# Kernel optimization log

Measured on AMD Instinct MI355X. Metric: run time of the kernel, lower is better.

Reference implementation:

```python
import jax, jax.numpy as jnp
import numpy as np

N = 8192
DIMS = [1024, 512, 256, 128]
ALPHA, BETA, ETA = 100.0, 1.0, 25.0


def setup_inputs() -> dict:
    key = jax.random.key(0)
    ks = jax.random.split(key, 20)
    X = jax.random.normal(ks[0], (N, DIMS[0]), dtype=jnp.float32)
    adj = (jax.random.uniform(ks[1], (N, N)) < 0.005).astype(jnp.float32)

    def xavier(k, fan_in, fan_out):
        lim = jnp.sqrt(6.0 / (fan_in + fan_out))
        return jax.random.uniform(k, (fan_in, fan_out), minval=-lim, maxval=lim, dtype=jnp.float32)

    # encoder GraphConv params
    W0 = xavier(ks[2], DIMS[0], DIMS[1]); b0 = jnp.zeros((DIMS[1],), jnp.float32)
    W1 = xavier(ks[3], DIMS[1], DIMS[2]); b1 = jnp.zeros((DIMS[2],), jnp.float32)
    W2 = xavier(ks[4], DIMS[2], DIMS[3]); b2 = jnp.zeros((DIMS[3],), jnp.float32)
    # attn_head params (out_sz = DIMS[2] = 256, input dim = DIMS[2])
    attn_W = jax.random.normal(ks[5], (DIMS[2], DIMS[2]), dtype=jnp.float32)  # [out_sz, D], used as seq @ W.T
    attn_a1 = jax.random.normal(ks[6], (DIMS[2],), dtype=jnp.float32)
    attn_a2 = jax.random.normal(ks[7], (DIMS[2],), dtype=jnp.float32)
    # decoder params (struct reversed: 128->256->512->1024)
    rd = DIMS[::-1]
    dW0 = jax.random.normal(ks[8], (rd[0], rd[1]), dtype=jnp.float32); db0 = jnp.zeros((rd[1],), jnp.float32)
    dW1 = jax.random.normal(ks[9], (rd[1], rd[2]), dtype=jnp.float32); db1 = jnp.zeros((rd[2],), jnp.float32)
    dW2 = jax.random.normal(ks[10], (rd[2], rd[3]), dtype=jnp.float32); db2 = jnp.zeros((rd[3],), jnp.float32)
    return {"X": X, "adj": adj, "W0": W0, "b0": b0, "W1": W1, "b1": b1, "W2": W2, "b2": b2,
            "attn_W": attn_W, "attn_a1": attn_a1, "attn_a2": attn_a2,
            "dW0": dW0, "db0": db0, "dW1": dW1, "db1": db1, "dW2": dW2, "db2": db2}


def reference(X, adj, W0, b0, W1, b1, W2, b2, attn_W, attn_a1, attn_a2,
              dW0, db0, dW1, db1, dW2, db2):
    lrelu = jax.nn.leaky_relu  # negative_slope=0.01, matches torch default

    # --- encode (dropout disabled / eval-mode) ---
    h = lrelu(adj @ (X @ W0) + b0)          # [N, 512]
    h = lrelu(adj @ (h @ W1) + b1)          # [N, 256]

    # GAT-style attn head (out_sz = 256)
    seq_fts = h @ attn_W.T                  # [N, 256]
    f1 = seq_fts @ attn_a1                  # [N]
    f2 = seq_fts @ attn_a2                  # [N]
    logits = f1[:, None] + f2[None, :]      # [N, N]
    mask = (adj > 0).astype(seq_fts.dtype)
    masked = lrelu(logits) - 1e9 * (1.0 - mask)
    coefs = jax.nn.softmax(masked, axis=-1)
    h = lrelu(coefs @ seq_fts)              # [N, 256]

    H = lrelu(adj @ (h @ W2) + b2)          # [N, 128]

    # --- decode ---
    Xr = jax.nn.sigmoid(H @ dW0 + db0)
    Xr = jax.nn.sigmoid(Xr @ dW1 + db1)
    Xr = jax.nn.sigmoid(Xr @ dW2 + db2)     # [N, 1024]

    # --- losses ---
    deg = adj.sum(axis=1)
    LH = deg[:, None] * H - adj @ H         # (D - A) @ H without materializing D
    loss_emb = 2.0 * jnp.sum(H * LH)
    B = X * (ETA - 1.0) + 1.0
    loss_res = jnp.sum(((Xr - X) * B) ** 2)
    loss = ALPHA * loss_res + BETA * loss_emb
    return loss, H, Xr
```

## Files before the change

kernel.cpp:

```cpp
#include <hip/hip_runtime.h>
#include <math.h>

#define NN 8192
#define ELL_W 128

typedef __attribute__((ext_vector_type(8))) short bf16x8;
typedef __attribute__((ext_vector_type(4))) float f32x4;

__device__ __forceinline__ float lrelu(float x) { return x > 0.f ? x : 0.01f * x; }
__device__ __forceinline__ unsigned short f2bf(float f) {
    unsigned u = __float_as_uint(f);
    return (unsigned short)((u + 0x7FFFu + ((u >> 16) & 1u)) >> 16);
}
__device__ __forceinline__ float bf2f(unsigned short h) { return __uint_as_float(((unsigned)h) << 16); }
__device__ __forceinline__ void split3(float v, unsigned short& h0, unsigned short& h1, unsigned short& h2) {
    h0 = f2bf(v); float r = v - bf2f(h0);
    h1 = f2bf(r); h2 = f2bf(r - bf2f(h1));
}

__device__ __forceinline__ void gload_lds16(const unsigned short* g, unsigned short* l) {
    __builtin_amdgcn_global_load_lds((const __attribute__((address_space(1))) unsigned int*)g,
                                     (__attribute__((address_space(3))) unsigned int*)l, 16, 0, 0);
}

__device__ __forceinline__ size_t a_plane_off(int rowg, int kg, int K) {
    int rr = rowg & 127, kk = kg & 31;
    int pc = (((kk >> 3) + (rr >> 1)) & 3);
    return ((size_t)(rowg >> 7) * (K >> 5) + (kg >> 5)) * 4096 + rr * 32 + pc * 8 + (kk & 7);
}

__global__ void build_ell_kernel(const float* __restrict__ adj, int* __restrict__ ell,
                                 int* __restrict__ cnt, float* __restrict__ deg) {
    const int row  = blockIdx.x * 4 + (threadIdx.x >> 6);
    const int lane = threadIdx.x & 63;
    const float4* arow = (const float4*)(adj + (size_t)row * NN);
    const unsigned long long lmask = (1ull << lane) - 1ull;
    int count = 0;
    for (int c0 = 0; c0 < NN; c0 += 256) {
        const float4 v = arow[(c0 >> 2) + lane];
        const int col = c0 + lane * 4;
        float f[4] = {v.x, v.y, v.z, v.w};
        #pragma unroll
        for (int q = 0; q < 4; ++q) {
            unsigned long long m = __ballot(f[q] > 0.f);
            if (f[q] > 0.f) {
                int pos = count + __popcll(m & lmask);
                if (pos < ELL_W) ell[row * ELL_W + pos] = col + q;
            }
            count += __popcll(m);
        }
    }
    if (lane == 0) {
        cnt[row] = count < ELL_W ? count : ELL_W;
        deg[row] = (float)count;
    }
}

__global__ void zero_accum_kernel(float* accum) { accum[0] = 0.f; accum[1] = 0.f; }

__global__ void splitA_kernel(const float* __restrict__ src, unsigned short* __restrict__ P0,
                              unsigned short* __restrict__ P1, unsigned short* __restrict__ P2,
                              int K, int nchunks) {
    int g = blockIdx.x * 256 + threadIdx.x;
    if (g >= nchunks) return;
    const int KT = K >> 5;
    int t = g >> 9, w = g & 511;
    int r = w >> 2, pc = w & 3;
    int c = (pc - (r >> 1)) & 3;
    int tm = t / KT, tk = t % KT;
    const float* s = src + (size_t)(tm * 128 + r) * K + tk * 32 + c * 8;
    const float4 v0 = *(const float4*)s, v1 = *(const float4*)(s + 4);
    float f[8] = {v0.x, v0.y, v0.z, v0.w, v1.x, v1.y, v1.z, v1.w};
    unsigned short a0[8], a1[8], a2[8];
    #pragma unroll
    for (int j = 0; j < 8; ++j) split3(f[j], a0[j], a1[j], a2[j]);
    *(uint4*)(P0 + (size_t)g * 8) = *(uint4*)a0;
    *(uint4*)(P1 + (size_t)g * 8) = *(uint4*)a1;
    *(uint4*)(P2 + (size_t)g * 8) = *(uint4*)a2;
}

__global__ void splitBT_kernel(const float* __restrict__ W, unsigned short* __restrict__ P0,
                               unsigned short* __restrict__ P1, unsigned short* __restrict__ P2,
                               int K, int N, int nchunks) {
    int g = blockIdx.x * 256 + threadIdx.x;
    if (g >= nchunks) return;
    const int KT = K >> 5;
    int t = g >> 8, w = g & 255;
    int r = w >> 2, pc = w & 3;
    int c = (pc - (r >> 1)) & 3;
    int tn = t / KT, tk = t % KT;
    const float* s = W + (size_t)(tk * 32 + c * 8) * N + tn * 64 + r;
    unsigned short a0[8], a1[8], a2[8];
    #pragma unroll
    for (int j = 0; j < 8; ++j) split3(s[(size_t)j * N], a0[j], a1[j], a2[j]);
    *(uint4*)(P0 + (size_t)g * 8) = *(uint4*)a0;
    *(uint4*)(P1 + (size_t)g * 8) = *(uint4*)a1;
    *(uint4*)(P2 + (size_t)g * 8) = *(uint4*)a2;
}

__global__ void splitBR_kernel(const float* __restrict__ W, unsigned short* __restrict__ P0,
                               unsigned short* __restrict__ P1, unsigned short* __restrict__ P2,
                               int K, int nchunks) {
    int g = blockIdx.x * 256 + threadIdx.x;
    if (g >= nchunks) return;
    const int KT = K >> 5;
    int t = g >> 8, w = g & 255;
    int r = w >> 2, pc = w & 3;
    int c = (pc - (r >> 1)) & 3;
    int tn = t / KT, tk = t % KT;
    const float* s = W + (size_t)(tn * 64 + r) * K + tk * 32 + c * 8;
    const float4 v0 = *(const float4*)s, v1 = *(const float4*)(s + 4);
    float f[8] = {v0.x, v0.y, v0.z, v0.w, v1.x, v1.y, v1.z, v1.w};
    unsigned short a0[8], a1[8], a2[8];
    #pragma unroll
    for (int j = 0; j < 8; ++j) split3(f[j], a0[j], a1[j], a2[j]);
    *(uint4*)(P0 + (size_t)g * 8) = *(uint4*)a0;
    *(uint4*)(P1 + (size_t)g * 8) = *(uint4*)a1;
    *(uint4*)(P2 + (size_t)g * 8) = *(uint4*)a2;
}

template <int ACT, int OUT>
__launch_bounds__(256)
__global__ void mfma_gemm_kernel(const unsigned short* __restrict__ A0, const unsigned short* __restrict__ A1,
                                 const unsigned short* __restrict__ A2,
                                 const unsigned short* __restrict__ B0, const unsigned short* __restrict__ B1,
                                 const unsigned short* __restrict__ B2,
                                 const float* __restrict__ bias, int K, int N,
                                 float* __restrict__ Cf,
                                 unsigned short* __restrict__ C0, unsigned short* __restrict__ C1,
                                 unsigned short* __restrict__ C2,
                                 const float* __restrict__ Xref, float* __restrict__ accum) {
    __shared__ __align__(16) unsigned short lds[18432];
    __shared__ float sred[256];
    const int tid = threadIdx.x, lane = tid & 63, wv = tid >> 6;
    const int KT = K >> 5;
    const int bm = blockIdx.y * 128, bn = blockIdx.x * 64;
    const int wr = (wv >> 1) * 64, wc = (wv & 1) * 32;
    const int lr = lane & 15, cch = lane >> 4;

    const unsigned short* Ap[3] = {A0 + (size_t)blockIdx.y * KT * 4096,
                                   A1 + (size_t)blockIdx.y * KT * 4096,
                                   A2 + (size_t)blockIdx.y * KT * 4096};
    const unsigned short* Bp[3] = {B0 + (size_t)blockIdx.x * KT * 2048,
                                   B1 + (size_t)blockIdx.x * KT * 2048,
                                   B2 + (size_t)blockIdx.x * KT * 2048};
    int offA[4], offB[2];
    #pragma unroll
    for (int mi = 0; mi < 4; ++mi) { int r = wr + mi * 16 + lr; offA[mi] = r * 32 + (((cch + (r >> 1)) & 3) << 3); }
    #pragma unroll
    for (int ni = 0; ni < 2; ++ni) { int r = wc + ni * 16 + lr; offB[ni] = r * 32 + (((cch + (r >> 1)) & 3) << 3); }

    f32x4 acc[4][2];
    #pragma unroll
    for (int i = 0; i < 4; ++i)
        #pragma unroll
        for (int j = 0; j < 2; ++j) acc[i][j] = (f32x4){0.f, 0.f, 0.f, 0.f};

    for (int tk = 0; tk < KT; ++tk) {
        #pragma unroll
        for (int i = 0; i < 6; ++i) {
            int s = i * 4 + wv, p = s >> 3, q = s & 7;
            gload_lds16(Ap[p] + (size_t)tk * 4096 + q * 512 + lane * 8, &lds[p * 4096 + q * 512]);
        }
        #pragma unroll
        for (int i = 0; i < 3; ++i) {
            int s = i * 4 + wv, p = s >> 2, q = s & 3;
            gload_lds16(Bp[p] + (size_t)tk * 2048 + q * 512 + lane * 8, &lds[12288 + p * 2048 + q * 512]);
        }
        __syncthreads();
        bf16x8 af[3][4], bfr[3][2];
        #pragma unroll
        for (int p = 0; p < 3; ++p) {
            #pragma unroll
            for (int mi = 0; mi < 4; ++mi) af[p][mi] = *(const bf16x8*)&lds[p * 4096 + offA[mi]];
            #pragma unroll
            for (int ni = 0; ni < 2; ++ni) bfr[p][ni] = *(const bf16x8*)&lds[12288 + p * 2048 + offB[ni]];
        }
        #pragma unroll
        for (int mi = 0; mi < 4; ++mi)
            #pragma unroll
            for (int ni = 0; ni < 2; ++ni) {
                f32x4 c = acc[mi][ni];
                c = __builtin_amdgcn_mfma_f32_16x16x32_bf16(af[0][mi], bfr[0][ni], c, 0, 0, 0);
                c = __builtin_amdgcn_mfma_f32_16x16x32_bf16(af[0][mi], bfr[1][ni], c, 0, 0, 0);
                c = __builtin_amdgcn_mfma_f32_16x16x32_bf16(af[1][mi], bfr[0][ni], c, 0, 0, 0);
                c = __builtin_amdgcn_mfma_f32_16x16x32_bf16(af[1][mi], bfr[1][ni], c, 0, 0, 0);
                c = __builtin_amdgcn_mfma_f32_16x16x32_bf16(af[0][mi], bfr[2][ni], c, 0, 0, 0);
                c = __builtin_amdgcn_mfma_f32_16x16x32_bf16(af[2][mi], bfr[0][ni], c, 0, 0, 0);
                acc[mi][ni] = c;
            }
        __syncthreads();
    }
    float local = 0.f;
    #pragma unroll
    for (int mi = 0; mi < 4; ++mi)
        #pragma unroll
        for (int ni = 0; ni < 2; ++ni) {
            const int colg = bn + wc + ni * 16 + lr;
            #pragma unroll
            for (int r = 0; r < 4; ++r) {
                const int rowg = bm + wr + mi * 16 + cch * 4 + r;
                float v = acc[mi][ni][r];
                if (ACT) { v += bias[colg]; v = 1.f / (1.f + __expf(-v)); }
                if (OUT == 0) {
                    Cf[(size_t)rowg * N + colg] = v;
                } else if (OUT == 1) {
                    size_t po = a_plane_off(rowg, colg, N);
                    unsigned short h0, h1, h2; split3(v, h0, h1, h2);
                    C0[po] = h0; C1[po] = h1; C2[po] = h2;
                } else {
                    const size_t o = (size_t)rowg * N + colg;
                    Cf[o] = v;
                    float x = Xref[o];
                    float d = (v - x) * fmaf(x, 24.f, 1.f);
                    local = fmaf(d, d, local);
                }
            }
        }
    if (OUT == 2) {
        sred[tid] = local; __syncthreads();
        for (int s = 128; s; s >>= 1) { if (tid < s) sred[tid] += sred[tid + s]; __syncthreads(); }
        if (tid == 0) atomicAdd(accum, sred[0]);
    }
}

template <int C, int OUTF, int OUTP>
__global__ void spmm_kernel(const float* __restrict__ M_, const int* __restrict__ ell,
                            const int* __restrict__ cnt, const float* __restrict__ bias,
                            float* __restrict__ out, float* __restrict__ out2,
                            unsigned short* __restrict__ P0, unsigned short* __restrict__ P1,
                            unsigned short* __restrict__ P2) {
    constexpr int TPR = C / 4;
    constexpr int RPB = 256 / TPR;
    const int rid = threadIdx.x / TPR;
    const int c4  = threadIdx.x % TPR;
    const int row = blockIdx.x * RPB + rid;
    __shared__ int nb_s[RPB][ELL_W];
    const int n = cnt[row];
    for (int t = c4; t < n; t += TPR) nb_s[rid][t] = ell[row * ELL_W + t];
    __syncthreads();
    float4 acc = {0.f, 0.f, 0.f, 0.f};
    for (int t = 0; t < n; ++t) {
        const float4 v = *(const float4*)(M_ + (size_t)nb_s[rid][t] * C + c4 * 4);
        acc.x += v.x; acc.y += v.y; acc.z += v.z; acc.w += v.w;
    }
    const float4 bv = *(const float4*)(bias + c4 * 4);
    float4 r;
    r.x = lrelu(acc.x + bv.x); r.y = lrelu(acc.y + bv.y);
    r.z = lrelu(acc.z + bv.z); r.w = lrelu(acc.w + bv.w);
    if (OUTF) {
        *(float4*)(out + (size_t)row * C + c4 * 4) = r;
        if (out2) {
            size_t o = (size_t)row * C + c4 * 4;
            out2[o] = r.x; out2[o + 1] = r.y; out2[o + 2] = r.z; out2[o + 3] = r.w;
        }
    }
    if (OUTP) {
        constexpr int KT = C >> 5;
        int tm = row >> 7, rr = row & 127;
        int tk = c4 >> 3, cc = (c4 >> 1) & 3, h = c4 & 1;
        int pc = (cc + (rr >> 1)) & 3;
        size_t off = ((size_t)tm * KT + tk) * 4096 + rr * 32 + pc * 8 + h * 4;
        ushort4 q0, q1, q2;
        split3(r.x, q0.x, q1.x, q2.x); split3(r.y, q0.y, q1.y, q2.y);
        split3(r.z, q0.z, q1.z, q2.z); split3(r.w, q0.w, q1.w, q2.w);
        *(ushort4*)(P0 + off) = q0; *(ushort4*)(P1 + off) = q1; *(ushort4*)(P2 + off) = q2;
    }
}

__global__ void f12_kernel(const float* __restrict__ seq, const float* __restrict__ a1,
                           const float* __restrict__ a2, float* __restrict__ f1,
                           float* __restrict__ f2) {
    const int row = blockIdx.x * 4 + (threadIdx.x >> 6);
    const int lane = threadIdx.x & 63;
    const float4 v  = *(const float4*)(seq + (size_t)row * 256 + lane * 4);
    const float4 w1 = *(const float4*)(a1 + lane * 4);
    const float4 w2 = *(const float4*)(a2 + lane * 4);
    float s1 = v.x * w1.x + v.y * w1.y + v.z * w1.z + v.w * w1.w;
    float s2 = v.x * w2.x + v.y * w2.y + v.z * w2.z + v.w * w2.w;
    #pragma unroll
    for (int o = 32; o; o >>= 1) { s1 += __shfl_xor(s1, o); s2 += __shfl_xor(s2, o); }
    if (lane == 0) { f1[row] = s1; f2[row] = s2; }
}

__global__ void attn_kernel(const float* __restrict__ seq, const int* __restrict__ ell,
                            const int* __restrict__ cnt, const float* __restrict__ f1,
                            const float* __restrict__ f2,
                            unsigned short* __restrict__ P0, unsigned short* __restrict__ P1,
                            unsigned short* __restrict__ P2) {
    const int wid = threadIdx.x >> 6, lane = threadIdx.x & 63;
    const int row = blockIdx.x * 4 + wid;
    __shared__ int   nb_s[4][ELL_W];
    __shared__ float cf_s[4][ELL_W];
    const int n = cnt[row];
    const float f1r = f1[row];
    float m = -3.0e38f;
    for (int t = lane; t < n; t += 64) {
        int j = ell[row * ELL_W + t];
        nb_s[wid][t] = j;
        float v = lrelu(f1r + f2[j]);
        cf_s[wid][t] = v;
        m = fmaxf(m, v);
    }
    #pragma unroll
    for (int o = 32; o; o >>= 1) m = fmaxf(m, __shfl_xor(m, o));
    __syncthreads();
    float s = 0.f;
    for (int t = lane; t < n; t += 64) {
        float e = __expf(cf_s[wid][t] - m);
        cf_s[wid][t] = e;
        s += e;
    }
    #pragma unroll
    for (int o = 32; o; o >>= 1) s += __shfl_xor(s, o);
    const float inv = 1.f / s;
    __syncthreads();
    float4 acc = {0.f, 0.f, 0.f, 0.f};
    for (int t = 0; t < n; ++t) {
        const float c = cf_s[wid][t];
        const float4 v = *(const float4*)(seq + (size_t)nb_s[wid][t] * 256 + lane * 4);
        acc.x = fmaf(c, v.x, acc.x); acc.y = fmaf(c, v.y, acc.y);
        acc.z = fmaf(c, v.z, acc.z); acc.w = fmaf(c, v.w, acc.w);
    }
    float4 r;
    r.x = lrelu(acc.x * inv); r.y = lrelu(acc.y * inv);
    r.z = lrelu(acc.z * inv); r.w = lrelu(acc.w * inv);
    int tm = row >> 7, rr = row & 127;
    int tk = lane >> 3, cc = (lane >> 1) & 3, h = lane & 1;
    int pc = (cc + (rr >> 1)) & 3;
    size_t off = ((size_t)tm * 8 + tk) * 4096 + rr * 32 + pc * 8 + h * 4;
    ushort4 q0, q1, q2;
    split3(r.x, q0.x, q1.x, q2.x); split3(r.y, q0.y, q1.y, q2.y);
    split3(r.z, q0.z, q1.z, q2.z); split3(r.w, q0.w, q1.w, q2.w);
    *(ushort4*)(P0 + off) = q0; *(ushort4*)(P1 + off) = q1; *(ushort4*)(P2 + off) = q2;
}

__global__ void loss_emb_kernel(const float* __restrict__ H, const int* __restrict__ ell,
                                const int* __restrict__ cnt, const float* __restrict__ deg,
                                float* __restrict__ accum) {
    const int row = blockIdx.x, tid = threadIdx.x;
    __shared__ int nb[ELL_W];
    __shared__ float sred[128];
    const int n = cnt[row];
    if (tid < n) nb[tid] = ell[row * ELL_W + tid];
    __syncthreads();
    float hv = H[(size_t)row * 128 + tid];
    float g = 0.f;
    for (int t = 0; t < n; ++t) g += H[(size_t)nb[t] * 128 + tid];
    float lh = deg[row] * hv - g;
    sred[tid] = hv * lh; __syncthreads();
    for (int s = 64; s; s >>= 1) { if (tid < s) sred[tid] += sred[tid + s]; __syncthreads(); }
    if (tid == 0) atomicAdd(accum + 1, sred[0]);
}

__global__ void finalize_kernel(const float* __restrict__ accum, float* __restrict__ out) {
    out[0] = 100.f * accum[0] + 2.f * accum[1];
}

extern "C" void kernel_launch(void* const* d_in, const int* in_sizes, int n_in,
                              void* d_out, int out_size, void* d_ws, size_t ws_size,
                              hipStream_t stream) {
    const float* X      = (const float*)d_in[0];
    const float* adj    = (const float*)d_in[1];
    const float* W0     = (const float*)d_in[2];
    const float* b0     = (const float*)d_in[3];
    const float* W1     = (const float*)d_in[4];
    const float* b1     = (const float*)d_in[5];
    const float* W2     = (const float*)d_in[6];
    const float* b2     = (const float*)d_in[7];
    const float* attn_W = (const float*)d_in[8];
    const float* a1     = (const float*)d_in[9];
    const float* a2     = (const float*)d_in[10];
    const float* dW0    = (const float*)d_in[11];
    const float* db0    = (const float*)d_in[12];
    const float* dW1    = (const float*)d_in[13];
    const float* db1    = (const float*)d_in[14];
    const float* dW2    = (const float*)d_in[15];
    const float* db2    = (const float*)d_in[16];

    float* out  = (float*)d_out;
    float* Hout = out + 1;
    float* Xr   = out + 1 + (size_t)NN * 128;

    char* w = (char*)d_ws;
    int*   ell   = (int*)w;   w += (size_t)NN * ELL_W * 4;
    int*   cnt   = (int*)w;   w += (size_t)NN * 4;
    float* deg   = (float*)w; w += (size_t)NN * 4;
    float* f1    = (float*)w; w += (size_t)NN * 4;
    float* f2    = (float*)w; w += (size_t)NN * 4;
    float* accum = (float*)w; w += 256;
    float* bufA  = (float*)w; w += (size_t)NN * 512 * 4;
    float* bufB  = (float*)w; w += (size_t)NN * 256 * 4;
    float* bufC  = (float*)w; w += (size_t)NN * 256 * 4;
    float* bufH  = (float*)w; w += (size_t)NN * 128 * 4;
    unsigned short *XP[3], *W0T[3], *h0P[3], *W1T[3], *h1P[3], *aWR[3], *h2P[3], *W2T[3];
    unsigned short *HP[3], *dW0T[3], *R0P[3], *dW1T[3], *R1P[3], *dW2T[3];
    for (int i = 0; i < 3; ++i) { XP[i]   = (unsigned short*)w; w += (size_t)NN * 1024 * 2; }
    for (int i = 0; i < 3; ++i) { W0T[i]  = (unsigned short*)w; w += (size_t)512 * 1024 * 2; }
    for (int i = 0; i < 3; ++i) { h0P[i]  = (unsigned short*)w; w += (size_t)NN * 512 * 2; }
    for (int i = 0; i < 3; ++i) { W1T[i]  = (unsigned short*)w; w += (size_t)256 * 512 * 2; }
    for (int i = 0; i < 3; ++i) { h1P[i]  = (unsigned short*)w; w += (size_t)NN * 256 * 2; }
    for (int i = 0; i < 3; ++i) { aWR[i]  = (unsigned short*)w; w += (size_t)256 * 256 * 2; }
    for (int i = 0; i < 3; ++i) { h2P[i]  = (unsigned short*)w; w += (size_t)NN * 256 * 2; }
    for (int i = 0; i < 3; ++i) { W2T[i]  = (unsigned short*)w; w += (size_t)128 * 256 * 2; }
    for (int i = 0; i < 3; ++i) { HP[i]   = (unsigned short*)w; w += (size_t)NN * 128 * 2; }
    for (int i = 0; i < 3; ++i) { dW0T[i] = (unsigned short*)w; w += (size_t)256 * 128 * 2; }
    for (int i = 0; i < 3; ++i) { R0P[i]  = (unsigned short*)w; w += (size_t)NN * 256 * 2; }
    for (int i = 0; i < 3; ++i) { dW1T[i] = (unsigned short*)w; w += (size_t)512 * 256 * 2; }
    for (int i = 0; i < 3; ++i) { R1P[i]  = (unsigned short*)w; w += (size_t)NN * 512 * 2; }
    for (int i = 0; i < 3; ++i) { dW2T[i] = (unsigned short*)w; w += (size_t)1024 * 512 * 2; }

    build_ell_kernel<<<dim3(NN / 4), dim3(256), 0, stream>>>(adj, ell, cnt, deg);
    zero_accum_kernel<<<1, 1, 0, stream>>>(accum);

    splitA_kernel<<<4096, 256, 0, stream>>>(X, XP[0], XP[1], XP[2], 1024, NN * 1024 / 8);
    splitBT_kernel<<<256, 256, 0, stream>>>(W0, W0T[0], W0T[1], W0T[2], 1024, 512, 512 * 1024 / 8);
    splitBT_kernel<<<64, 256, 0, stream>>>(W1, W1T[0], W1T[1], W1T[2], 512, 256, 256 * 512 / 8);
    splitBR_kernel<<<32, 256, 0, stream>>>(attn_W, aWR[0], aWR[1], aWR[2], 256, 256 * 256 / 8);
    splitBT_kernel<<<16, 256, 0, stream>>>(W2, W2T[0], W2T[1], W2T[2], 256, 128, 128 * 256 / 8);
    splitBT_kernel<<<16, 256, 0, stream>>>(dW0, dW0T[0], dW0T[1], dW0T[2], 128, 256, 256 * 128 / 8);
    splitBT_kernel<<<64, 256, 0, stream>>>(dW1, dW1T[0], dW1T[1], dW1T[2], 256, 512, 512 * 256 / 8);
    splitBT_kernel<<<256, 256, 0, stream>>>(dW2, dW2T[0], dW2T[1], dW2T[2], 512, 1024, 1024 * 512 / 8);

    mfma_gemm_kernel<0, 0><<<dim3(8, 64), 256, 0, stream>>>(
        XP[0], XP[1], XP[2], W0T[0], W0T[1], W0T[2], nullptr, 1024, 512,
        bufA, nullptr, nullptr, nullptr, nullptr, nullptr);
    spmm_kernel<512, 0, 1><<<NN / 2, 256, 0, stream>>>(bufA, ell, cnt, b0, nullptr, nullptr, h0P[0], h0P[1], h0P[2]);
    mfma_gemm_kernel<0, 0><<<dim3(4, 64), 256, 0, stream>>>(
        h0P[0], h0P[1], h0P[2], W1T[0], W1T[1], W1T[2], nullptr, 512, 256,
        bufC, nullptr, nullptr, nullptr, nullptr, nullptr);
    spmm_kernel<256, 0, 1><<<NN / 4, 256, 0, stream>>>(bufC, ell, cnt, b1, nullptr, nullptr, h1P[0], h1P[1], h1P[2]);
    mfma_gemm_kernel<0, 0><<<dim3(4, 64), 256, 0, stream>>>(
        h1P[0], h1P[1], h1P[2], aWR[0], aWR[1], aWR[2], nullptr, 256, 256,
        bufB, nullptr, nullptr, nullptr, nullptr, nullptr);
    f12_kernel<<<NN / 4, 256, 0, stream>>>(bufB, a1, a2, f1, f2);
    attn_kernel<<<NN / 4, 256, 0, stream>>>(bufB, ell, cnt, f1, f2, h2P[0], h2P[1], h2P[2]);
    mfma_gemm_kernel<0, 0><<<dim3(2, 64), 256, 0, stream>>>(
        h2P[0], h2P[1], h2P[2], W2T[0], W2T[1], W2T[2], nullptr, 256, 128,
        bufA, nullptr, nullptr, nullptr, nullptr, nullptr);
    spmm_kernel<128, 1, 1><<<NN / 8, 256, 0, stream>>>(bufA, ell, cnt, b2, bufH, Hout, HP[0], HP[1], HP[2]);
    mfma_gemm_kernel<1, 1><<<dim3(4, 64), 256, 0, stream>>>(
        HP[0], HP[1], HP[2], dW0T[0], dW0T[1], dW0T[2], db0, 128, 256,
        nullptr, R0P[0], R0P[1], R0P[2], nullptr, nullptr);
    mfma_gemm_kernel<1, 1><<<dim3(8, 64), 256, 0, stream>>>(
        R0P[0], R0P[1], R0P[2], dW1T[0], dW1T[1], dW1T[2], db1, 256, 512,
        nullptr, R1P[0], R1P[1], R1P[2], nullptr, nullptr);
    mfma_gemm_kernel<1, 2><<<dim3(16, 64), 256, 0, stream>>>(
        R1P[0], R1P[1], R1P[2], dW2T[0], dW2T[1], dW2T[2], db2, 512, 1024,
        Xr, nullptr, nullptr, nullptr, X, accum);
    loss_emb_kernel<<<NN, 128, 0, stream>>>(bufH, ell, cnt, deg, accum);
    finalize_kernel<<<1, 1, 0, stream>>>(accum, out);
}
```

Measured before the change: 929.4 us.

## Switch GEMM emulation from three-way bf16 split to two-way scaled fp16 split

Fp32 GEMM operands are now split into two fp16 planes instead of three bf16 planes. Each tile needs three MFMAs instead of six, and plane storage and traffic drop by a third. Activations from spmm and attention are pre-scaled by 1/64 to stay in fp16 range, and the GEMM epilogue rescales. The GEMM also gains a TM template for 64-row tiles on the narrower GEMMs and an XCD-aware block remap. Values are clamped to ±60000, and fp16's smaller exponent range risks underflow or overflow in the low-order plane, which can hurt accuracy.

```diff
diff --git a/kernel.cpp b/kernel.cpp
--- a/kernel.cpp
+++ b/kernel.cpp
@@ -3,19 +3,20 @@
 
 #define NN 8192
 #define ELL_W 128
-
-typedef __attribute__((ext_vector_type(8))) short bf16x8;
+#define ASCL 0.015625f
+
+typedef _Float16 f16x8 __attribute__((ext_vector_type(8)));
 typedef __attribute__((ext_vector_type(4))) float f32x4;
 
 __device__ __forceinline__ float lrelu(float x) { return x > 0.f ? x : 0.01f * x; }
-__device__ __forceinline__ unsigned short f2bf(float f) {
-    unsigned u = __float_as_uint(f);
-    return (unsigned short)((u + 0x7FFFu + ((u >> 16) & 1u)) >> 16);
-}
-__device__ __forceinline__ float bf2f(unsigned short h) { return __uint_as_float(((unsigned)h) << 16); }
-__device__ __forceinline__ void split3(float v, unsigned short& h0, unsigned short& h1, unsigned short& h2) {
-    h0 = f2bf(v); float r = v - bf2f(h0);
-    h1 = f2bf(r); h2 = f2bf(r - bf2f(h1));
+
+__device__ __forceinline__ void split2(float v, unsigned short& u0, unsigned short& u1) {
+    v = fminf(fmaxf(v, -60000.f), 60000.f);
+    _Float16 a = (_Float16)v;
+    float r = v - (float)a;
+    _Float16 b = (_Float16)r;
+    u0 = *(unsigned short*)&a;
+    u1 = *(unsigned short*)&b;
 }
 
 __device__ __forceinline__ void gload_lds16(const unsigned short* g, unsigned short* l) {
@@ -59,8 +60,7 @@
 __global__ void zero_accum_kernel(float* accum) { accum[0] = 0.f; accum[1] = 0.f; }
 
 __global__ void splitA_kernel(const float* __restrict__ src, unsigned short* __restrict__ P0,
-                              unsigned short* __restrict__ P1, unsigned short* __restrict__ P2,
-                              int K, int nchunks) {
+                              unsigned short* __restrict__ P1, int K, int nchunks) {
     int g = blockIdx.x * 256 + threadIdx.x;
     if (g >= nchunks) return;
     const int KT = K >> 5;
@@ -71,17 +71,15 @@
     const float* s = src + (size_t)(tm * 128 + r) * K + tk * 32 + c * 8;
     const float4 v0 = *(const float4*)s, v1 = *(const float4*)(s + 4);
     float f[8] = {v0.x, v0.y, v0.z, v0.w, v1.x, v1.y, v1.z, v1.w};
-    unsigned short a0[8], a1[8], a2[8];
-    #pragma unroll
-    for (int j = 0; j < 8; ++j) split3(f[j], a0[j], a1[j], a2[j]);
+    unsigned short a0[8], a1[8];
+    #pragma unroll
+    for (int j = 0; j < 8; ++j) split2(f[j], a0[j], a1[j]);
     *(uint4*)(P0 + (size_t)g * 8) = *(uint4*)a0;
     *(uint4*)(P1 + (size_t)g * 8) = *(uint4*)a1;
-    *(uint4*)(P2 + (size_t)g * 8) = *(uint4*)a2;
 }
 
 __global__ void splitBT_kernel(const float* __restrict__ W, unsigned short* __restrict__ P0,
-                               unsigned short* __restrict__ P1, unsigned short* __restrict__ P2,
-                               int K, int N, int nchunks) {
+                               unsigned short* __restrict__ P1, int K, int N, int nchunks) {
     int g = blockIdx.x * 256 + threadIdx.x;
     if (g >= nchunks) return;
     const int KT = K >> 5;
@@ -90,17 +88,15 @@
     int c = (pc - (r >> 1)) & 3;
     int tn = t / KT, tk = t % KT;
     const float* s = W + (size_t)(tk * 32 + c * 8) * N + tn * 64 + r;
-    unsigned short a0[8], a1[8], a2[8];
-    #pragma unroll
-    for (int j = 0; j < 8; ++j) split3(s[(size_t)j * N], a0[j], a1[j], a2[j]);
+    unsigned short a0[8], a1[8];
+    #pragma unroll
+    for (int j = 0; j < 8; ++j) split2(s[(size_t)j * N], a0[j], a1[j]);
     *(uint4*)(P0 + (size_t)g * 8) = *(uint4*)a0;
     *(uint4*)(P1 + (size_t)g * 8) = *(uint4*)a1;
-    *(uint4*)(P2 + (size_t)g * 8) = *(uint4*)a2;
 }
 
 __global__ void splitBR_kernel(const float* __restrict__ W, unsigned short* __restrict__ P0,
-                               unsigned short* __restrict__ P1, unsigned short* __restrict__ P2,
-                               int K, int nchunks) {
+                               unsigned short* __restrict__ P1, int K, int nchunks) {
     int g = blockIdx.x * 256 + threadIdx.x;
     if (g >= nchunks) return;
     const int KT = K >> 5;
@@ -111,103 +107,100 @@
     const float* s = W + (size_t)(tn * 64 + r) * K + tk * 32 + c * 8;
     const float4 v0 = *(const float4*)s, v1 = *(const float4*)(s + 4);
     float f[8] = {v0.x, v0.y, v0.z, v0.w, v1.x, v1.y, v1.z, v1.w};
-    unsigned short a0[8], a1[8], a2[8];
-    #pragma unroll
-    for (int j = 0; j < 8; ++j) split3(f[j], a0[j], a1[j], a2[j]);
+    unsigned short a0[8], a1[8];
+    #pragma unroll
+    for (int j = 0; j < 8; ++j) split2(f[j], a0[j], a1[j]);
     *(uint4*)(P0 + (size_t)g * 8) = *(uint4*)a0;
     *(uint4*)(P1 + (size_t)g * 8) = *(uint4*)a1;
-    *(uint4*)(P2 + (size_t)g * 8) = *(uint4*)a2;
-}
-
-template <int ACT, int OUT>
+}
+
+template <int TM, int ACT, int OUT>
 __launch_bounds__(256)
 __global__ void mfma_gemm_kernel(const unsigned short* __restrict__ A0, const unsigned short* __restrict__ A1,
-                                 const unsigned short* __restrict__ A2,
                                  const unsigned short* __restrict__ B0, const unsigned short* __restrict__ B1,
-                                 const unsigned short* __restrict__ B2,
-                                 const float* __restrict__ bias, int K, int N,
+                                 const float* __restrict__ bias, int K, int N, float ascale,
                                  float* __restrict__ Cf,
                                  unsigned short* __restrict__ C0, unsigned short* __restrict__ C1,
-                                 unsigned short* __restrict__ C2,
                                  const float* __restrict__ Xref, float* __restrict__ accum) {
-    __shared__ __align__(16) unsigned short lds[18432];
-    __shared__ float sred[256];
+    constexpr int MI  = TM / 32;
+    constexpr int APL = TM * 32;
+    constexpr int ASEG = TM / 16;
+    __shared__ __align__(16) unsigned short lds[2 * APL + 4096];
     const int tid = threadIdx.x, lane = tid & 63, wv = tid >> 6;
     const int KT = K >> 5;
-    const int bm = blockIdx.y * 128, bn = blockIdx.x * 64;
-    const int wr = (wv >> 1) * 64, wc = (wv & 1) * 32;
+    const int nx = gridDim.x;
+    const int id = blockIdx.y * nx + blockIdx.x;
+    const int cpx = (nx * gridDim.y) >> 3;
+    const int lid = (id & 7) * cpx + (id >> 3);
+    const int bxx = lid % nx, byy = lid / nx;
+    const int bm = byy * TM, bn = bxx * 64;
+    const int wr = (wv >> 1) * (TM / 2), wc = (wv & 1) * 32;
     const int lr = lane & 15, cch = lane >> 4;
 
-    const unsigned short* Ap[3] = {A0 + (size_t)blockIdx.y * KT * 4096,
-                                   A1 + (size_t)blockIdx.y * KT * 4096,
-                                   A2 + (size_t)blockIdx.y * KT * 4096};
-    const unsigned short* Bp[3] = {B0 + (size_t)blockIdx.x * KT * 2048,
-                                   B1 + (size_t)blockIdx.x * KT * 2048,
-                                   B2 + (size_t)blockIdx.x * KT * 2048};
-    int offA[4], offB[2];
-    #pragma unroll
-    for (int mi = 0; mi < 4; ++mi) { int r = wr + mi * 16 + lr; offA[mi] = r * 32 + (((cch + (r >> 1)) & 3) << 3); }
+    const size_t abase = (size_t)(bm >> 7) * KT * 4096 + (bm & 127) * 32;
+    const unsigned short* Ap[2] = {A0 + abase, A1 + abase};
+    const unsigned short* Bp[2] = {B0 + (size_t)bxx * KT * 2048, B1 + (size_t)bxx * KT * 2048};
+    int offA[MI], offB[2];
+    #pragma unroll
+    for (int mi = 0; mi < MI; ++mi) { int r = wr + mi * 16 + lr; offA[mi] = r * 32 + (((cch + (r >> 1)) & 3) << 3); }
     #pragma unroll
     for (int ni = 0; ni < 2; ++ni) { int r = wc + ni * 16 + lr; offB[ni] = r * 32 + (((cch + (r >> 1)) & 3) << 3); }
 
-    f32x4 acc[4][2];
-    #pragma unroll
-    for (int i = 0; i < 4; ++i)
+    f32x4 acc[MI][2];
+    #pragma unroll
+    for (int i = 0; i < MI; ++i)
         #pragma unroll
         for (int j = 0; j < 2; ++j) acc[i][j] = (f32x4){0.f, 0.f, 0.f, 0.f};
 
     for (int tk = 0; tk < KT; ++tk) {
         #pragma unroll
-        for (int i = 0; i < 6; ++i) {
-            int s = i * 4 + wv, p = s >> 3, q = s & 7;
-            gload_lds16(Ap[p] + (size_t)tk * 4096 + q * 512 + lane * 8, &lds[p * 4096 + q * 512]);
-        }
-        #pragma unroll
-        for (int i = 0; i < 3; ++i) {
+        for (int i = 0; i < 2 * ASEG / 4; ++i) {
+            int s = i * 4 + wv, p = s / ASEG, q = s % ASEG;
+            gload_lds16(Ap[p] + (size_t)tk * 4096 + q * 512 + lane * 8, &lds[p * APL + q * 512]);
+        }
+        #pragma unroll
+        for (int i = 0; i < 2; ++i) {
             int s = i * 4 + wv, p = s >> 2, q = s & 3;
-            gload_lds16(Bp[p] + (size_t)tk * 2048 + q * 512 + lane * 8, &lds[12288 + p * 2048 + q * 512]);
+            gload_lds16(Bp[p] + (size_t)tk * 2048 + q * 512 + lane * 8, &lds[2 * APL + p * 2048 + q * 512]);
         }
         __syncthreads();
-        bf16x8 af[3][4], bfr[3][2];
-        #pragma unroll
-        for (int p = 0; p < 3; ++p) {
+        f16x8 af[2][MI], bfr[2][2];
+        #pragma unroll
+        for (int p = 0; p < 2; ++p) {
             #pragma unroll
-            for (int mi = 0; mi < 4; ++mi) af[p][mi] = *(const bf16x8*)&lds[p * 4096 + offA[mi]];
+            for (int mi = 0; mi < MI; ++mi) af[p][mi] = *(const f16x8*)&lds[p * APL + offA[mi]];
             #pragma unroll
-            for (int ni = 0; ni < 2; ++ni) bfr[p][ni] = *(const bf16x8*)&lds[12288 + p * 2048 + offB[ni]];
-        }
-        #pragma unroll
-        for (int mi = 0; mi < 4; ++mi)
+            for (int ni = 0; ni < 2; ++ni) bfr[p][ni] = *(const f16x8*)&lds[2 * APL + p * 2048 + offB[ni]];
+        }
+        #pragma unroll
+        for (int mi = 0; mi < MI; ++mi)
             #pragma unroll
             for (int ni = 0; ni < 2; ++ni) {
                 f32x4 c = acc[mi][ni];
-                c = __builtin_amdgcn_mfma_f32_16x16x32_bf16(af[0][mi], bfr[0][ni], c, 0, 0, 0);
-                c = __builtin_amdgcn_mfma_f32_16x16x32_bf16(af[0][mi], bfr[1][ni], c, 0, 0, 0);
-                c = __builtin_amdgcn_mfma_f32_16x16x32_bf16(af[1][mi], bfr[0][ni], c, 0, 0, 0);
-                c = __builtin_amdgcn_mfma_f32_16x16x32_bf16(af[1][mi], bfr[1][ni], c, 0, 0, 0);
-                c = __builtin_amdgcn_mfma_f32_16x16x32_bf16(af[0][mi], bfr[2][ni], c, 0, 0, 0);
-                c = __builtin_amdgcn_mfma_f32_16x16x32_bf16(af[2][mi], bfr[0][ni], c, 0, 0, 0);
+                c = __builtin_amdgcn_mfma_f32_16x16x32_f16(af[0][mi], bfr[0][ni], c, 0, 0, 0);
+                c = __builtin_amdgcn_mfma_f32_16x16x32_f16(af[0][mi], bfr[1][ni], c, 0, 0, 0);
+                c = __builtin_amdgcn_mfma_f32_16x16x32_f16(af[1][mi], bfr[0][ni], c, 0, 0, 0);
                 acc[mi][ni] = c;
             }
         __syncthreads();
     }
     float local = 0.f;
     #pragma unroll
-    for (int mi = 0; mi < 4; ++mi)
+    for (int mi = 0; mi < MI; ++mi)
         #pragma unroll
         for (int ni = 0; ni < 2; ++ni) {
             const int colg = bn + wc + ni * 16 + lr;
             #pragma unroll
             for (int r = 0; r < 4; ++r) {
                 const int rowg = bm + wr + mi * 16 + cch * 4 + r;
-                float v = acc[mi][ni][r];
+                float v = acc[mi][ni][r] * ascale;
                 if (ACT) { v += bias[colg]; v = 1.f / (1.f + __expf(-v)); }
                 if (OUT == 0) {
                     Cf[(size_t)rowg * N + colg] = v;
                 } else if (OUT == 1) {
                     size_t po = a_plane_off(rowg, colg, N);
-                    unsigned short h0, h1, h2; split3(v, h0, h1, h2);
-                    C0[po] = h0; C1[po] = h1; C2[po] = h2;
+                    unsigned short h0, h1; split2(v, h0, h1);
+                    C0[po] = h0; C1[po] = h1;
                 } else {
                     const size_t o = (size_t)rowg * N + colg;
                     Cf[o] = v;
@@ -218,6 +211,7 @@
             }
         }
     if (OUT == 2) {
+        float* sred = (float*)lds;
         sred[tid] = local; __syncthreads();
         for (int s = 128; s; s >>= 1) { if (tid < s) sred[tid] += sred[tid + s]; __syncthreads(); }
         if (tid == 0) atomicAdd(accum, sred[0]);
@@ -228,8 +222,7 @@
 __global__ void spmm_kernel(const float* __restrict__ M_, const int* __restrict__ ell,
                             const int* __restrict__ cnt, const float* __restrict__ bias,
                             float* __restrict__ out, float* __restrict__ out2,
-                            unsigned short* __restrict__ P0, unsigned short* __restrict__ P1,
-                            unsigned short* __restrict__ P2) {
+                            unsigned short* __restrict__ P0, unsigned short* __restrict__ P1) {
     constexpr int TPR = C / 4;
     constexpr int RPB = 256 / TPR;
     const int rid = threadIdx.x / TPR;
@@ -261,10 +254,10 @@
         int tk = c4 >> 3, cc = (c4 >> 1) & 3, h = c4 & 1;
         int pc = (cc + (rr >> 1)) & 3;
         size_t off = ((size_t)tm * KT + tk) * 4096 + rr * 32 + pc * 8 + h * 4;
-        ushort4 q0, q1, q2;
-        split3(r.x, q0.x, q1.x, q2.x); split3(r.y, q0.y, q1.y, q2.y);
-        split3(r.z, q0.z, q1.z, q2.z); split3(r.w, q0.w, q1.w, q2.w);
-        *(ushort4*)(P0 + off) = q0; *(ushort4*)(P1 + off) = q1; *(ushort4*)(P2 + off) = q2;
+        ushort4 q0, q1;
+        split2(r.x * ASCL, q0.x, q1.x); split2(r.y * ASCL, q0.y, q1.y);
+        split2(r.z * ASCL, q0.z, q1.z); split2(r.w * ASCL, q0.w, q1.w);
+        *(ushort4*)(P0 + off) = q0; *(ushort4*)(P1 + off) = q1;
     }
 }
 
@@ -286,8 +279,7 @@
 __global__ void attn_kernel(const float* __restrict__ seq, const int* __restrict__ ell,
                             const int* __restrict__ cnt, const float* __restrict__ f1,
                             const float* __restrict__ f2,
-                            unsigned short* __restrict__ P0, unsigned short* __restrict__ P1,
-                            unsigned short* __restrict__ P2) {
+                            unsigned short* __restrict__ P0, unsigned short* __restrict__ P1) {
     const int wid = threadIdx.x >> 6, lane = threadIdx.x & 63;
     const int row = blockIdx.x * 4 + wid;
     __shared__ int   nb_s[4][ELL_W];
@@ -329,10 +321,10 @@
     int tk = lane >> 3, cc = (lane >> 1) & 3, h = lane & 1;
     int pc = (cc + (rr >> 1)) & 3;
     size_t off = ((size_t)tm * 8 + tk) * 4096 + rr * 32 + pc * 8 + h * 4;
-    ushort4 q0, q1, q2;
-    split3(r.x, q0.x, q1.x, q2.x); split3(r.y, q0.y, q1.y, q2.y);
-    split3(r.z, q0.z, q1.z, q2.z); split3(r.w, q0.w, q1.w, q2.w);
-    *(ushort4*)(P0 + off) = q0; *(ushort4*)(P1 + off) = q1; *(ushort4*)(P2 + off) = q2;
+    ushort4 q0, q1;
+    split2(r.x * ASCL, q0.x, q1.x); split2(r.y * ASCL, q0.y, q1.y);
+    split2(r.z * ASCL, q0.z, q1.z); split2(r.w * ASCL, q0.w, q1.w);
+    *(ushort4*)(P0 + off) = q0; *(ushort4*)(P1 + off) = q1;
 }
 
 __global__ void loss_emb_kernel(const float* __restrict__ H, const int* __restrict__ ell,
@@ -393,61 +385,54 @@
     float* bufB  = (float*)w; w += (size_t)NN * 256 * 4;
     float* bufC  = (float*)w; w += (size_t)NN * 256 * 4;
     float* bufH  = (float*)w; w += (size_t)NN * 128 * 4;
-    unsigned short *XP[3], *W0T[3], *h0P[3], *W1T[3], *h1P[3], *aWR[3], *h2P[3], *W2T[3];
-    unsigned short *HP[3], *dW0T[3], *R0P[3], *dW1T[3], *R1P[3], *dW2T[3];
-    for (int i = 0; i < 3; ++i) { XP[i]   = (unsigned short*)w; w += (size_t)NN * 1024 * 2; }
-    for (int i = 0; i < 3; ++i) { W0T[i]  = (unsigned short*)w; w += (size_t)512 * 1024 * 2; }
-    for (int i = 0; i < 3; ++i) { h0P[i]  = (unsigned short*)w; w += (size_t)NN * 512 * 2; }
-    for (int i = 0; i < 3; ++i) { W1T[i]  = (unsigned short*)w; w += (size_t)256 * 512 * 2; }
-    for (int i = 0; i < 3; ++i) { h1P[i]  = (unsigned short*)w; w += (size_t)NN * 256 * 2; }
-    for (int i = 0; i < 3; ++i) { aWR[i]  = (unsigned short*)w; w += (size_t)256 * 256 * 2; }
-    for (int i = 0; i < 3; ++i) { h2P[i]  = (unsigned short*)w; w += (size_t)NN * 256 * 2; }
-    for (int i = 0; i < 3; ++i) { W2T[i]  = (unsigned short*)w; w += (size_t)128 * 256 * 2; }
-    for (int i = 0; i < 3; ++i) { HP[i]   = (unsigned short*)w; w += (size_t)NN * 128 * 2; }
-    for (int i = 0; i < 3; ++i) { dW0T[i] = (unsigned short*)w; w += (size_t)256 * 128 * 2; }
-    for (int i = 0; i < 3; ++i) { R0P[i]  = (unsigned short*)w; w += (size_t)NN * 256 * 2; }
-    for (int i = 0; i < 3; ++i) { dW1T[i] = (unsigned short*)w; w += (size_t)512 * 256 * 2; }
-    for (int i = 0; i < 3; ++i) { R1P[i]  = (unsigned short*)w; w += (size_t)NN * 512 * 2; }
-    for (int i = 0; i < 3; ++i) { dW2T[i] = (unsigned short*)w; w += (size_t)1024 * 512 * 2; }
+    unsigned short *XP[2], *W0T[2], *h0P[2], *W1T[2], *h1P[2], *aWR[2], *h2P[2], *W2T[2];
+    unsigned short *HP[2], *dW0T[2], *R0P[2], *dW1T[2], *R1P[2], *dW2T[2];
+    for (int i = 0; i < 2; ++i) { XP[i]   = (unsigned short*)w; w += (size_t)NN * 1024 * 2; }
+    for (int i = 0; i < 2; ++i) { W0T[i]  = (unsigned short*)w; w += (size_t)512 * 1024 * 2; }
+    for (int i = 0; i < 2; ++i) { h0P[i]  = (unsigned short*)w; w += (size_t)NN * 512 * 2; }
+    for (int i = 0; i < 2; ++i) { W1T[i]  = (unsigned short*)w; w += (size_t)256 * 512 * 2; }
+    for (int i = 0; i < 2; ++i) { h1P[i]  = (unsigned short*)w; w += (size_t)NN * 256 * 2; }
+    for (int i = 0; i < 2; ++i) { aWR[i]  = (unsigned short*)w; w += (size_t)256 * 256 * 2; }
+    for (int i = 0; i < 2; ++i) { h2P[i]  = (unsigned short*)w; w += (size_t)NN * 256 * 2; }
+    for (int i = 0; i < 2; ++i) { W2T[i]  = (unsigned short*)w; w += (size_t)128 * 256 * 2; }
+    for (int i = 0; i < 2; ++i) { HP[i]   = (unsigned short*)w; w += (size_t)NN * 128 * 2; }
+    for (int i = 0; i < 2; ++i) { dW0T[i] = (unsigned short*)w; w += (size_t)256 * 128 * 2; }
+    for (int i = 0; i < 2; ++i) { R0P[i]  = (unsigned short*)w; w += (size_t)NN * 256 * 2; }
+    for (int i = 0; i < 2; ++i) { dW1T[i] = (unsigned short*)w; w += (size_t)512 * 256 * 2; }
+    for (int i = 0; i < 2; ++i) { R1P[i]  = (unsigned short*)w; w += (size_t)NN * 512 * 2; }
+    for (int i = 0; i < 2; ++i) { dW2T[i] = (unsigned short*)w; w += (size_t)1024 * 512 * 2; }
 
     build_ell_kernel<<<dim3(NN / 4), dim3(256), 0, stream>>>(adj, ell, cnt, deg);
     zero_accum_kernel<<<1, 1, 0, stream>>>(accum);
 
-    splitA_kernel<<<4096, 256, 0, stream>>>(X, XP[0], XP[1], XP[2], 1024, NN * 1024 / 8);
-    splitBT_kernel<<<256, 256, 0, stream>>>(W0, W0T[0], W0T[1], W0T[2], 1024, 512, 512 * 1024 / 8);
-    splitBT_kernel<<<64, 256, 0, stream>>>(W1, W1T[0], W1T[1], W1T[2], 512, 256, 256 * 512 / 8);
-    splitBR_kernel<<<32, 256, 0, stream>>>(attn_W, aWR[0], aWR[1], aWR[2], 256, 256 * 256 / 8);
-    splitBT_kernel<<<16, 256, 0, stream>>>(W2, W2T[0], W2T[1], W2T[2], 256, 128, 128 * 256 / 8);
-    splitBT_kernel<<<16, 256, 0, stream>>>(dW0, dW0T[0], dW0T[1], dW0T[2], 128, 256, 256 * 128 / 8);
-    splitBT_kernel<<<64, 256, 0, stream>>>(dW1, dW1T[0], dW1T[1], dW1T[2], 256, 512, 512 * 256 / 8);
-    splitBT_kernel<<<256, 256, 0, stream>>>(dW2, dW2T[0], dW2T[1], dW2T[2], 512, 1024, 1024 * 512 / 8);
-
-    mfma_gemm_kernel<0, 0><<<dim3(8, 64), 256, 0, stream>>>(
-        XP[0], XP[1], XP[2], W0T[0], W0T[1], W0T[2], nullptr, 1024, 512,
-        bufA, nullptr, nullptr, nullptr, nullptr, nullptr);
-    spmm_kernel<512, 0, 1><<<NN / 2, 256, 0, stream>>>(bufA, ell, cnt, b0, nullptr, nullptr, h0P[0], h0P[1], h0P[2]);
-    mfma_gemm_kernel<0, 0><<<dim3(4, 64), 256, 0, stream>>>(
-        h0P[0], h0P[1], h0P[2], W1T[0], W1T[1], W1T[2], nullptr, 512, 256,
-        bufC, nullptr, nullptr, nullptr, nullptr, nullptr);
-    spmm_kernel<256, 0, 1><<<NN / 4, 256, 0, stream>>>(bufC, ell, cnt, b1, nullptr, nullptr, h1P[0], h1P[1], h1P[2]);
-    mfma_gemm_kernel<0, 0><<<dim3(4, 64), 256, 0, stream>>>(
-        h1P[0], h1P[1], h1P[2], aWR[0], aWR[1], aWR[2], nullptr, 256, 256,
-        bufB, nullptr, nullptr, nullptr, nullptr, nullptr);
+    splitA_kernel<<<4096, 256, 0, stream>>>(X, XP[0], XP[1], 1024, NN * 1024 / 8);
+    splitBT_kernel<<<256, 256, 0, stream>>>(W0, W0T[0], W0T[1], 1024, 512, 512 * 1024 / 8);
+    splitBT_kernel<<<64, 256, 0, stream>>>(W1, W1T[0], W1T[1], 512, 256, 256 * 512 / 8);
+    splitBR_kernel<<<32, 256, 0, stream>>>(attn_W, aWR[0], aWR[1], 256, 256 * 256 / 8);
+    splitBT_kernel<<<16, 256, 0, stream>>>(W2, W2T[0], W2T[1], 256, 128, 128 * 256 / 8);
+    splitBT_kernel<<<16, 256, 0, stream>>>(dW0, dW0T[0], dW0T[1], 128, 256, 256 * 128 / 8);
+    splitBT_kernel<<<64, 256, 0, stream>>>(dW1, dW1T[0], dW1T[1], 256, 512, 512 * 256 / 8);
+    splitBT_kernel<<<256, 256, 0, stream>>>(dW2, dW2T[0], dW2T[1], 512, 1024, 1024 * 512 / 8);
+
+    mfma_gemm_kernel<128, 0, 0><<<dim3(8, 64), 256, 0, stream>>>(
+        XP[0], XP[1], W0T[0], W0T[1], nullptr, 1024, 512, 1.f, bufA, nullptr, nullptr, nullptr, nullptr);
+    spmm_kernel<512, 0, 1><<<NN / 2, 256, 0, stream>>>(bufA, ell, cnt, b0, nullptr, nullptr, h0P[0], h0P[1]);
+    mfma_gemm_kernel<64, 0, 0><<<dim3(4, 128), 256, 0, stream>>>(
+        h0P[0], h0P[1], W1T[0], W1T[1], nullptr, 512, 256, 64.f, bufC, nullptr, nullptr, nullptr, nullptr);
+    spmm_kernel<256, 0, 1><<<NN / 4, 256, 0, stream>>>(bufC, ell, cnt, b1, nullptr, nullptr, h1P[0], h1P[1]);
+    mfma_gemm_kernel<64, 0, 0><<<dim3(4, 128), 256, 0, stream>>>(
+        h1P[0], h1P[1], aWR[0], aWR[1], nullptr, 256, 256, 64.f, bufB, nullptr, nullptr, nullptr, nullptr);
     f12_kernel<<<NN / 4, 256, 0, stream>>>(bufB, a1, a2, f1, f2);
-    attn_kernel<<<NN / 4, 256, 0, stream>>>(bufB, ell, cnt, f1, f2, h2P[0], h2P[1], h2P[2]);
-    mfma_gemm_kernel<0, 0><<<dim3(2, 64), 256, 0, stream>>>(
-        h2P[0], h2P[1], h2P[2], W2T[0], W2T[1], W2T[2], nullptr, 256, 128,
-        bufA, nullptr, nullptr, nullptr, nullptr, nullptr);
-    spmm_kernel<128, 1, 1><<<NN / 8, 256, 0, stream>>>(bufA, ell, cnt, b2, bufH, Hout, HP[0], HP[1], HP[2]);
-    mfma_gemm_kernel<1, 1><<<dim3(4, 64), 256, 0, stream>>>(
-        HP[0], HP[1], HP[2], dW0T[0], dW0T[1], dW0T[2], db0, 128, 256,
-        nullptr, R0P[0], R0P[1], R0P[2], nullptr, nullptr);
-    mfma_gemm_kernel<1, 1><<<dim3(8, 64), 256, 0, stream>>>(
-        R0P[0], R0P[1], R0P[2], dW1T[0], dW1T[1], dW1T[2], db1, 256, 512,
-        nullptr, R1P[0], R1P[1], R1P[2], nullptr, nullptr);
-    mfma_gemm_kernel<1, 2><<<dim3(16, 64), 256, 0, stream>>>(
-        R1P[0], R1P[1], R1P[2], dW2T[0], dW2T[1], dW2T[2], db2, 512, 1024,
-        Xr, nullptr, nullptr, nullptr, X, accum);
+    attn_kernel<<<NN / 4, 256, 0, stream>>>(bufB, ell, cnt, f1, f2, h2P[0], h2P[1]);
+    mfma_gemm_kernel<64, 0, 0><<<dim3(2, 128), 256, 0, stream>>>(
+        h2P[0], h2P[1], W2T[0], W2T[1], nullptr, 256, 128, 64.f, bufA, nullptr, nullptr, nullptr, nullptr);
+    spmm_kernel<128, 1, 1><<<NN / 8, 256, 0, stream>>>(bufA, ell, cnt, b2, bufH, Hout, HP[0], HP[1]);
+    mfma_gemm_kernel<64, 1, 1><<<dim3(4, 128), 256, 0, stream>>>(
+        HP[0], HP[1], dW0T[0], dW0T[1], db0, 128, 256, 64.f, nullptr, R0P[0], R0P[1], nullptr, nullptr);
+    mfma_gemm_kernel<128, 1, 1><<<dim3(8, 64), 256, 0, stream>>>(
+        R0P[0], R0P[1], dW1T[0], dW1T[1], db1, 256, 512, 1.f, nullptr, R1P[0], R1P[1], nullptr, nullptr);
+    mfma_gemm_kernel<128, 1, 2><<<dim3(16, 64), 256, 0, stream>>>(
+        R1P[0], R1P[1], dW2T[0], dW2T[1], db2, 512, 1024, 1.f, Xr, nullptr, nullptr, X, accum);
     loss_emb_kernel<<<NN, 128, 0, stream>>>(bufH, ell, cnt, deg, accum);
     finalize_kernel<<<1, 1, 0, stream>>>(accum, out);
 }
```

After: 828.7 us. 10.8% less time.
